# Kernel tuning notes

Measured on AMD Instinct MI355X. Metric: run time of the kernel, lower is better.

## Reference

```python
import jax, jax.numpy as jnp
import numpy as np

B, T, D = 4, 1024, 2048      # batch, tokens, d_model (= Linear out_features)
N, S, H = 8, 8, 8            # n_concepts, gate_rank, degen_rank
ETA = 1.0


def setup_inputs() -> dict:
    key = jax.random.key(0)
    ks = jax.random.split(key, 9)
    return {
        "x": jax.random.normal(ks[0], (B, T, D), jnp.float32),
        # selector params (kaiming-ish then / d_model^2 -> small); use /D for nontrivial values
        "select_weight": jax.random.normal(ks[1], (N, D, S), jnp.float32) / D,
        "select_mean_diff": jax.random.normal(ks[2], (N, D), jnp.float32) / D,
        "imp_center": jax.random.normal(ks[3], (N,), jnp.float32),
        "imp_slope": jax.random.normal(ks[4], (N,), jnp.float32) * 5.0,
        "lora_update": jax.random.normal(ks[5], (N, D, H), jnp.float32) * 0.02,
        "lora_degen": jax.random.normal(ks[6], (N, D, H), jnp.float32) * 0.02,
        "bias_w": jax.random.normal(ks[7], (N, D), jnp.float32) * 0.02,
        "debias_w": jax.random.normal(ks[8], (N, D), jnp.float32) * 0.02,
    }


def reference(x, select_weight, select_mean_diff, imp_center, imp_slope,
              lora_update, lora_degen, bias_w, debias_w):
    # ---- SimpleSelectorOutProp ----
    # x: [B,T,D]; x_diff: [B,N,T,D]  (x.unsqueeze(1) - mean_diff[None,:,None,:])
    x_diff = x[:, None, :, :] - select_mean_diff[None, :, None, :]
    x_diff = x_diff / jnp.linalg.norm(x_diff, axis=3, keepdims=True)
    # cont: [B,N,T,S] = einsum('nds,bntd->bnts')**2
    cont = jnp.einsum('nds,bntd->bnts', select_weight, x_diff) ** 2
    score = cont.sum(axis=-1)                                   # [B,N,T]
    gate = jax.nn.sigmoid(imp_slope[None, :, None] * (score - imp_center[None, :, None]))
    sel_scale = gate.max(axis=1)[..., None]                     # [B,T,1] (max over concepts)
    sel_idx = gate.argmax(axis=1)                               # [B,T] int (top-1 concept)

    # ---- top-1 concept gather + low-rank update ----
    debias = jnp.take(debias_w, sel_idx, axis=0)                # [B,T,D]
    bias = jnp.take(bias_w, sel_idx, axis=0)                    # [B,T,D]
    upd = jnp.take(lora_update, sel_idx, axis=0)                # [B,T,D,H]
    dgn = jnp.take(lora_degen, sel_idx, axis=0)                 # [B,T,D,H]

    x_debias = x - debias
    mod_x = jnp.einsum('btdh,btd->bth', upd, x_debias)          # [B,T,H]
    degen_up = jnp.einsum('btdh,bth->btd', dgn, mod_x)          # [B,T,D]
    mod_x_bias = ETA * (bias + degen_up)

    # gated residual blend: (1 - s) * x + s * mod_x_bias
    return (1.0 - sel_scale) * x + sel_scale * mod_x_bias
```

## Files before the change

### kernel.cpp

```cpp
#include <hip/hip_runtime.h>
#include <math.h>

typedef unsigned short u16;
typedef unsigned int   u32;
typedef unsigned long long u64;
typedef __attribute__((ext_vector_type(4))) unsigned short u16x4;
typedef __attribute__((ext_vector_type(8))) unsigned short bf16x8;
typedef __attribute__((ext_vector_type(8))) short sh8;
typedef __attribute__((ext_vector_type(4))) float f32x4;

#define BT     4096
#define D      2048
#define NC     8
#define NCOL   144
#define KSPLIT 8
#define KR     (D / KSPLIT)

__device__ __forceinline__ float bf2f(u16 v) {
    u32 u = ((u32)v) << 16;
    float f; __builtin_memcpy(&f, &u, 4); return f;
}
__device__ __forceinline__ u16 f2bf(float f) {
    u32 u; __builtin_memcpy(&u, &f, 4);
    u += 0x7fffu + ((u >> 16) & 1);
    return (u16)(u >> 16);
}

__device__ __forceinline__ int detect_fp32(const void* xv) {
    const u16* p = (const u16*)xv;
    int l = threadIdx.x & 63;
    bool bad = false;
#pragma unroll
    for (int i = 0; i < 4; i++) {
        float v = bf2f(p[l * 4 + i]);
        if (!(fabsf(v) < 1e4f)) bad = true;
    }
    return __ballot(bad) != 0ull;
}

template<int DT> struct IO;
template<> struct IO<0> {
    static __device__ __forceinline__ float ld1(const void* p, size_t i) {
        return bf2f(((const u16*)p)[i]);
    }
    static __device__ __forceinline__ void ld4(const void* p, size_t i, float* o) {
        u16x4 v = *(const u16x4*)((const u16*)p + i);
#pragma unroll
        for (int k = 0; k < 4; k++) o[k] = bf2f(v[k]);
    }
    static __device__ __forceinline__ void ld8(const void* p, size_t i, float* o) {
        bf16x8 v = *(const bf16x8*)((const u16*)p + i);
#pragma unroll
        for (int k = 0; k < 8; k++) o[k] = bf2f(v[k]);
    }
    static __device__ __forceinline__ void st4(void* p, size_t i, const float* v) {
        u16x4 o;
#pragma unroll
        for (int k = 0; k < 4; k++) o[k] = f2bf(v[k]);
        *(u16x4*)((u16*)p + i) = o;
    }
    static __device__ __forceinline__ u16 ldbf(const void* p, size_t i) {
        return ((const u16*)p)[i];
    }
    static __device__ __forceinline__ sh8 afrag(const void* p, size_t i) {
        return *(const sh8*)((const u16*)p + i);
    }
};
template<> struct IO<1> {
    static __device__ __forceinline__ float ld1(const void* p, size_t i) {
        return ((const float*)p)[i];
    }
    static __device__ __forceinline__ void ld4(const void* p, size_t i, float* o) {
        f32x4 a = *(const f32x4*)((const float*)p + i);
#pragma unroll
        for (int k = 0; k < 4; k++) o[k] = a[k];
    }
    static __device__ __forceinline__ void ld8(const void* p, size_t i, float* o) {
        f32x4 a = *(const f32x4*)((const float*)p + i);
        f32x4 b = *(const f32x4*)((const float*)p + i + 4);
#pragma unroll
        for (int k = 0; k < 4; k++) { o[k] = a[k]; o[4 + k] = b[k]; }
    }
    static __device__ __forceinline__ void st4(void* p, size_t i, const float* v) {
        f32x4 a;
#pragma unroll
        for (int k = 0; k < 4; k++) a[k] = v[k];
        *(f32x4*)((float*)p + i) = a;
    }
    static __device__ __forceinline__ u16 ldbf(const void* p, size_t i) {
        return f2bf(((const float*)p)[i]);
    }
    static __device__ __forceinline__ sh8 afrag(const void* p, size_t i) {
        f32x4 a = *(const f32x4*)((const float*)p + i);
        f32x4 b = *(const f32x4*)((const float*)p + i + 4);
        sh8 r;
#pragma unroll
        for (int k = 0; k < 4; k++) {
            r[k]     = (short)f2bf(a[k]);
            r[4 + k] = (short)f2bf(b[k]);
        }
        return r;
    }
};

template<int DT>
__device__ __forceinline__ void prep_part(const void* selW, const void* upd,
                                          const void* mu, u16* __restrict__ WtT) {
    int idx = blockIdx.x * 256 + threadIdx.x;
    int j = idx >> 8, d0 = (idx & 255) * 8;
    bf16x8 v;
    if (j < 64) {
        int n = j >> 3, s = j & 7;
#pragma unroll
        for (int i = 0; i < 8; i++) v[i] = IO<DT>::ldbf(selW, ((size_t)n * D + d0 + i) * 8 + s);
    } else if (j < 128) {
        int n = (j - 64) >> 3, h = j & 7;
#pragma unroll
        for (int i = 0; i < 8; i++) v[i] = IO<DT>::ldbf(upd, ((size_t)n * D + d0 + i) * 8 + h);
    } else if (j < 136) {
#pragma unroll
        for (int i = 0; i < 8; i++) v[i] = IO<DT>::ldbf(mu, (size_t)(j - 128) * D + d0 + i);
    } else {
#pragma unroll
        for (int i = 0; i < 8; i++) v[i] = 0;
    }
    *(bf16x8*)(WtT + (size_t)j * D + d0) = v;
}

template<int DT>
__device__ __forceinline__ void consts_part(const void* W, const void* mu,
                                            const void* upd, const void* deb,
                                            float* gOff, float* gMu2, float* gUb) {
    int bid = blockIdx.x - 144;
    int n = bid >> 3, t = threadIdx.x;
    int d = (bid & 7) * 256 + t;

    float mud = IO<DT>::ld1(mu,  (size_t)n * D + d);
    float dbd = IO<DT>::ld1(deb, (size_t)n * D + d);
    float m2 = mud * mud;
    float wv[8], uv[8], o[8], u[8];
    IO<DT>::ld8(W,   ((size_t)n * D + d) * 8, wv);
    IO<DT>::ld8(upd, ((size_t)n * D + d) * 8, uv);
#pragma unroll
    for (int s = 0; s < 8; s++) { o[s] = wv[s] * mud; u[s] = uv[s] * dbd; }

#pragma unroll
    for (int i = 1; i < 64; i <<= 1) {
        m2 += __shfl_xor(m2, i, 64);
#pragma unroll
        for (int s = 0; s < 8; s++) {
            o[s] += __shfl_xor(o[s], i, 64);
            u[s] += __shfl_xor(u[s], i, 64);
        }
    }
    __shared__ float red[4][17];
    int wave = t >> 6, lane = t & 63;
    if (lane == 0) {
        red[wave][0] = m2;
#pragma unroll
        for (int s = 0; s < 8; s++) { red[wave][1 + s] = o[s]; red[wave][9 + s] = u[s]; }
    }
    __syncthreads();
    if (t < 17) {
        float acc = red[0][t] + red[1][t] + red[2][t] + red[3][t];
        if (t == 0)      atomicAdd(&gMu2[n], acc);
        else if (t < 9)  atomicAdd(&gOff[n * 8 + t - 1], acc);
        else             atomicAdd(&gUb[n * 8 + t - 9], acc);
    }
}

template<int DT>
__device__ __forceinline__ void dgnb_part(const void* dgn, u16* __restrict__ dgnb) {
    int idx = (blockIdx.x - 208) * 256 + threadIdx.x;
    float v[8];
    IO<DT>::ld8(dgn, (size_t)idx * 8, v);
    bf16x8 o;
#pragma unroll
    for (int k = 0; k < 8; k++) o[k] = f2bf(v[k]);
    *(bf16x8*)(dgnb + (size_t)idx * 8) = o;
}

__global__ __launch_bounds__(256) void k_prep(
    const void* x, const void* selW, const void* upd, const void* mu,
    const void* deb, const void* dgn, u16* WtT,
    float* gOff, float* gMu2, float* gUb, u16* dgnb) {
    int f = detect_fp32(x);
    if (blockIdx.x < 144) {
        if (f) prep_part<1>(selW, upd, mu, WtT); else prep_part<0>(selW, upd, mu, WtT);
    } else if (blockIdx.x < 208) {
        if (f) consts_part<1>(selW, mu, upd, deb, gOff, gMu2, gUb);
        else   consts_part<0>(selW, mu, upd, deb, gOff, gMu2, gUb);
    } else {
        if (f) dgnb_part<1>(dgn, dgnb); else dgnb_part<0>(dgn, dgnb);
    }
}

template<int DT>
__device__ __forceinline__ void gemm_body(const void* X, const u16* __restrict__ WtT,
                                          float* __restrict__ Pslices,
                                          float* __restrict__ sumx2p) {
    const int t = threadIdx.x;
    const int w = t >> 6, l = t & 63;
    const int m = l & 15, q = l >> 4;
    const int tok0 = blockIdx.x * 64 + w * 16;
    const int p = blockIdx.y;
    const int k0 = p * KR;

    const size_t aoff = (size_t)(tok0 + m) * D + k0 + q * 8;
    const u16* bp = WtT + (size_t)m * D + k0 + q * 8;

    f32x4 acc[9];
#pragma unroll
    for (int ct = 0; ct < 9; ct++) acc[ct] = (f32x4){0.f, 0.f, 0.f, 0.f};
    float s2 = 0.f;

#pragma unroll 2
    for (int ks = 0; ks < KR / 32; ks++) {
        sh8 a = IO<DT>::afrag(X, aoff + ks * 32);
        sh8 b[9];
#pragma unroll
        for (int ct = 0; ct < 9; ct++)
            b[ct] = *(const sh8*)(bp + (size_t)ct * 16 * D + ks * 32);
#pragma unroll
        for (int i = 0; i < 8; i++) {
            float xv = bf2f((u16)a[i]);
            s2 = fmaf(xv, xv, s2);
        }
#pragma unroll
        for (int ct = 0; ct < 9; ct++)
            acc[ct] = __builtin_amdgcn_mfma_f32_16x16x32_bf16(a, b[ct], acc[ct], 0, 0, 0);
    }

    s2 += __shfl_xor(s2, 16, 64);
    s2 += __shfl_xor(s2, 32, 64);
    if (l < 16) sumx2p[(size_t)p * BT + tok0 + l] = s2;

    float* Ps = Pslices + (size_t)p * BT * NCOL;
#pragma unroll
    for (int ct = 0; ct < 9; ct++)
#pragma unroll
        for (int r = 0; r < 4; r++)
            Ps[(size_t)(tok0 + q * 4 + r) * NCOL + ct * 16 + m] = acc[ct][r];
}
__global__ __launch_bounds__(256) void k_gemm(const void* X, const u16* WtT,
                                              float* Pslices, float* sumx2p) {
    if (detect_fp32(X)) gemm_body<1>(X, WtT, Pslices, sumx2p);
    else                gemm_body<0>(X, WtT, Pslices, sumx2p);
}

template<int DT>
__device__ __forceinline__ void gate_body(
    const float* __restrict__ Pslices, const float* __restrict__ sumx2p,
    const void* CENTER, const void* SLOPE,
    const float* __restrict__ OFF, const float* __restrict__ MU2,
    const float* __restrict__ UB,
    float* __restrict__ svals, int* __restrict__ cs, float* __restrict__ mxs) {
    const int g = blockIdx.x * 256 + threadIdx.x;
    const int tok = g >> 3, n = g & 7;

    f32x4 pa = {0.f, 0.f, 0.f, 0.f}, pb = {0.f, 0.f, 0.f, 0.f};
    float mdot = 0.f, s2 = 0.f;
#pragma unroll
    for (int p = 0; p < KSPLIT; p++) {
        const float* pr = Pslices + ((size_t)p * BT + tok) * NCOL;
        f32x4 a = *(const f32x4*)(pr + 8 * n);
        f32x4 b = *(const f32x4*)(pr + 8 * n + 4);
#pragma unroll
        for (int k = 0; k < 4; k++) { pa[k] += a[k]; pb[k] += b[k]; }
        mdot += pr[128 + n];
        s2 += sumx2p[(size_t)p * BT + tok];
    }

    float norm2 = s2 - 2.f * mdot + MU2[n];
    float sc = 0.f;
#pragma unroll
    for (int s = 0; s < 4; s++) {
        float d0 = pa[s] - OFF[8 * n + s];
        float d1 = pb[s] - OFF[8 * n + 4 + s];
        sc += d0 * d0 + d1 * d1;
    }
    sc /= norm2;
    float zv = IO<DT>::ld1(SLOPE, n) * (sc - IO<DT>::ld1(CENTER, n));
    int iv = n;
#pragma unroll
    for (int i = 1; i < 8; i <<= 1) {
        float z2 = __shfl_xor(zv, i, 64);
        int   i2 = __shfl_xor(iv, i, 64);
        if (z2 > zv || (z2 == zv && i2 < iv)) { zv = z2; iv = i2; }
    }
    const int c = iv;
    float mxv = 0.f;
#pragma unroll
    for (int p = 0; p < KSPLIT; p++)
        mxv += Pslices[((size_t)p * BT + tok) * NCOL + 64 + 8 * c + n];
    mxs[(size_t)tok * 8 + n] = mxv - UB[c * 8 + n];
    if (n == 0) { svals[tok] = 1.f / (1.f + expf(-zv)); cs[tok] = c; }
}
__global__ __launch_bounds__(256) void k_gate(
    const float* Pslices, const float* sumx2p, const void* X,
    const void* CENTER, const void* SLOPE,
    const float* OFF, const float* MU2, const float* UB,
    float* svals, int* cs, float* mxs) {
    if (detect_fp32(X)) gate_body<1>(Pslices, sumx2p, CENTER, SLOPE, OFF, MU2, UB, svals, cs, mxs);
    else                gate_body<0>(Pslices, sumx2p, CENTER, SLOPE, OFF, MU2, UB, svals, cs, mxs);
}

template<int DT>
__device__ __forceinline__ void blend_body(
    const void* X, const float* __restrict__ svals, const int* __restrict__ cs,
    const float* __restrict__ mxs, const u16* __restrict__ DGNB,
    const void* BIAS, void* OUT) {
    const int tok = blockIdx.x >> 1;
    const int d0 = (blockIdx.x & 1) * 1024 + threadIdx.x * 4;

    const int c = cs[tok];
    const float sval = svals[tok];
    f32x4 mxa = *(const f32x4*)(mxs + (size_t)tok * 8);
    f32x4 mxb = *(const f32x4*)(mxs + (size_t)tok * 8 + 4);

    float xf[4], bv[4], ov[4];
    IO<DT>::ld4(X,    (size_t)tok * D + d0, xf);
    IO<DT>::ld4(BIAS, (size_t)c * D + d0, bv);
#pragma unroll
    for (int i = 0; i < 4; i++) {
        bf16x8 v = *(const bf16x8*)(DGNB + ((size_t)c * D + d0 + i) * 8);
        float du = bf2f(v[0]) * mxa[0] + bf2f(v[1]) * mxa[1]
                 + bf2f(v[2]) * mxa[2] + bf2f(v[3]) * mxa[3]
                 + bf2f(v[4]) * mxb[0] + bf2f(v[5]) * mxb[1]
                 + bf2f(v[6]) * mxb[2] + bf2f(v[7]) * mxb[3];
        ov[i] = (1.f - sval) * xf[i] + sval * (bv[i] + du);
    }
    IO<DT>::st4(OUT, (size_t)tok * D + d0, ov);
}
__global__ __launch_bounds__(256) void k_blend(
    const void* X, const float* svals, const int* cs, const float* mxs,
    const u16* DGNB, const void* BIAS, void* OUT) {
    if (detect_fp32(X)) blend_body<1>(X, svals, cs, mxs, DGNB, BIAS, OUT);
    else                blend_body<0>(X, svals, cs, mxs, DGNB, BIAS, OUT);
}

extern "C" void kernel_launch(void* const* d_in, const int* in_sizes, int n_in,
                              void* d_out, int out_size, void* d_ws, size_t ws_size,
                              hipStream_t stream) {
    const void* x      = d_in[0];
    const void* selW   = d_in[1];
    const void* mu     = d_in[2];
    const void* center = d_in[3];
    const void* slope  = d_in[4];
    const void* upd    = d_in[5];
    const void* dgn    = d_in[6];
    const void* biasW  = d_in[7];
    const void* debW   = d_in[8];

    float* Pslices = (float*)d_out;
    char* ws = (char*)d_ws;
    float* sumx2p = (float*)ws;
    float* svals  = (float*)(ws + 131072);
    int*   cs     = (int*)  (ws + 147456);
    float* mxs    = (float*)(ws + 163840);
    u16*   WtT    = (u16*)  (ws + 294912);
    u16*   dgnb   = (u16*)  (ws + 884736);
    float* consts = (float*)(ws + 1146880);
    float* off = consts, *mu2 = consts + 64, *ub = consts + 72;

    hipMemsetAsync(consts, 0, 576, stream);
    k_prep <<<272, 256, 0, stream>>>(x, selW, upd, mu, debW, dgn,
                                     WtT, off, mu2, ub, dgnb);
    k_gemm <<<dim3(BT / 64, KSPLIT), 256, 0, stream>>>(x, WtT, Pslices, sumx2p);
    k_gate <<<BT * NC / 256, 256, 0, stream>>>(Pslices, sumx2p, x, center, slope,
                                               off, mu2, ub, svals, cs, mxs);
    k_blend<<<BT * 2, 256, 0, stream>>>(x, svals, cs, mxs, dgnb, biasW, d_out);
}
```

Baseline: 143.4 us.

## Fuse gate into blend, store partial GEMM results as bf16, double K-split

```diff
diff --git a/kernel.cpp b/kernel.cpp
--- a/kernel.cpp
+++ b/kernel.cpp
@@ -13,7 +13,7 @@
 #define D      2048
 #define NC     8
 #define NCOL   144
-#define KSPLIT 8
+#define KSPLIT 16
 #define KR     (D / KSPLIT)
 
 __device__ __forceinline__ float bf2f(u16 v) {
@@ -131,19 +131,22 @@
 __device__ __forceinline__ void consts_part(const void* W, const void* mu,
                                             const void* upd, const void* deb,
                                             float* gOff, float* gMu2, float* gUb) {
-    int bid = blockIdx.x - 144;
-    int n = bid >> 3, t = threadIdx.x;
-    int d = (bid & 7) * 256 + t;
-
-    float mud = IO<DT>::ld1(mu,  (size_t)n * D + d);
-    float dbd = IO<DT>::ld1(deb, (size_t)n * D + d);
-    float m2 = mud * mud;
-    float wv[8], uv[8], o[8], u[8];
-    IO<DT>::ld8(W,   ((size_t)n * D + d) * 8, wv);
-    IO<DT>::ld8(upd, ((size_t)n * D + d) * 8, uv);
-#pragma unroll
-    for (int s = 0; s < 8; s++) { o[s] = wv[s] * mud; u[s] = uv[s] * dbd; }
-
+    int n = blockIdx.x - 144, t = threadIdx.x;
+    float o[8] = {}, u[8] = {};
+    float m2 = 0.f;
+    for (int d = t; d < D; d += 256) {
+        float mud = IO<DT>::ld1(mu,  (size_t)n * D + d);
+        float dbd = IO<DT>::ld1(deb, (size_t)n * D + d);
+        m2 += mud * mud;
+        float wv[8], uv[8];
+        IO<DT>::ld8(W,   ((size_t)n * D + d) * 8, wv);
+        IO<DT>::ld8(upd, ((size_t)n * D + d) * 8, uv);
+#pragma unroll
+        for (int s = 0; s < 8; s++) {
+            o[s] += wv[s] * mud;
+            u[s] += uv[s] * dbd;
+        }
+    }
 #pragma unroll
     for (int i = 1; i < 64; i <<= 1) {
         m2 += __shfl_xor(m2, i, 64);
@@ -161,17 +164,20 @@
         for (int s = 0; s < 8; s++) { red[wave][1 + s] = o[s]; red[wave][9 + s] = u[s]; }
     }
     __syncthreads();
-    if (t < 17) {
-        float acc = red[0][t] + red[1][t] + red[2][t] + red[3][t];
-        if (t == 0)      atomicAdd(&gMu2[n], acc);
-        else if (t < 9)  atomicAdd(&gOff[n * 8 + t - 1], acc);
-        else             atomicAdd(&gUb[n * 8 + t - 9], acc);
+    if (t == 0) {
+        float acc[17];
+#pragma unroll
+        for (int i = 0; i < 17; i++)
+            acc[i] = red[0][i] + red[1][i] + red[2][i] + red[3][i];
+        gMu2[n] = acc[0];
+#pragma unroll
+        for (int s = 0; s < 8; s++) { gOff[n * 8 + s] = acc[1 + s]; gUb[n * 8 + s] = acc[9 + s]; }
     }
 }
 
 template<int DT>
 __device__ __forceinline__ void dgnb_part(const void* dgn, u16* __restrict__ dgnb) {
-    int idx = (blockIdx.x - 208) * 256 + threadIdx.x;
+    int idx = (blockIdx.x - 152) * 256 + threadIdx.x;
     float v[8];
     IO<DT>::ld8(dgn, (size_t)idx * 8, v);
     bf16x8 o;
@@ -187,7 +193,7 @@
     int f = detect_fp32(x);
     if (blockIdx.x < 144) {
         if (f) prep_part<1>(selW, upd, mu, WtT); else prep_part<0>(selW, upd, mu, WtT);
-    } else if (blockIdx.x < 208) {
+    } else if (blockIdx.x < 152) {
         if (f) consts_part<1>(selW, mu, upd, deb, gOff, gMu2, gUb);
         else   consts_part<0>(selW, mu, upd, deb, gOff, gMu2, gUb);
     } else {
@@ -197,7 +203,7 @@
 
 template<int DT>
 __device__ __forceinline__ void gemm_body(const void* X, const u16* __restrict__ WtT,
-                                          float* __restrict__ Pslices,
+                                          u16* __restrict__ Pb,
                                           float* __restrict__ sumx2p) {
     const int t = threadIdx.x;
     const int w = t >> 6, l = t & 63;
@@ -214,7 +220,7 @@
     for (int ct = 0; ct < 9; ct++) acc[ct] = (f32x4){0.f, 0.f, 0.f, 0.f};
     float s2 = 0.f;
 
-#pragma unroll 2
+#pragma unroll
     for (int ks = 0; ks < KR / 32; ks++) {
         sh8 a = IO<DT>::afrag(X, aoff + ks * 32);
         sh8 b[9];
@@ -235,108 +241,169 @@
     s2 += __shfl_xor(s2, 32, 64);
     if (l < 16) sumx2p[(size_t)p * BT + tok0 + l] = s2;
 
-    float* Ps = Pslices + (size_t)p * BT * NCOL;
+    u16* Ps = Pb + (size_t)p * BT * NCOL;
 #pragma unroll
     for (int ct = 0; ct < 9; ct++)
 #pragma unroll
         for (int r = 0; r < 4; r++)
-            Ps[(size_t)(tok0 + q * 4 + r) * NCOL + ct * 16 + m] = acc[ct][r];
+            Ps[(size_t)(tok0 + q * 4 + r) * NCOL + ct * 16 + m] = f2bf(acc[ct][r]);
 }
 __global__ __launch_bounds__(256) void k_gemm(const void* X, const u16* WtT,
-                                              float* Pslices, float* sumx2p) {
-    if (detect_fp32(X)) gemm_body<1>(X, WtT, Pslices, sumx2p);
-    else                gemm_body<0>(X, WtT, Pslices, sumx2p);
-}
-
-template<int DT>
-__device__ __forceinline__ void gate_body(
-    const float* __restrict__ Pslices, const float* __restrict__ sumx2p,
-    const void* CENTER, const void* SLOPE,
+                                              u16* Pb, float* sumx2p) {
+    if (detect_fp32(X)) gemm_body<1>(X, WtT, Pb, sumx2p);
+    else                gemm_body<0>(X, WtT, Pb, sumx2p);
+}
+
+template<int DT>
+__device__ __forceinline__ void gate_wave(
+    const u16* __restrict__ Pb, const float* __restrict__ sumx2p,
+    int tok, int l, const void* CENTER, const void* SLOPE,
     const float* __restrict__ OFF, const float* __restrict__ MU2,
     const float* __restrict__ UB,
-    float* __restrict__ svals, int* __restrict__ cs, float* __restrict__ mxs) {
-    const int g = blockIdx.x * 256 + threadIdx.x;
-    const int tok = g >> 3, n = g & 7;
-
-    f32x4 pa = {0.f, 0.f, 0.f, 0.f}, pb = {0.f, 0.f, 0.f, 0.f};
-    float mdot = 0.f, s2 = 0.f;
-#pragma unroll
-    for (int p = 0; p < KSPLIT; p++) {
-        const float* pr = Pslices + ((size_t)p * BT + tok) * NCOL;
-        f32x4 a = *(const f32x4*)(pr + 8 * n);
-        f32x4 b = *(const f32x4*)(pr + 8 * n + 4);
-#pragma unroll
-        for (int k = 0; k < 4; k++) { pa[k] += a[k]; pb[k] += b[k]; }
-        mdot += pr[128 + n];
-        s2 += sumx2p[(size_t)p * BT + tok];
-    }
-
-    float norm2 = s2 - 2.f * mdot + MU2[n];
-    float sc = 0.f;
-#pragma unroll
-    for (int s = 0; s < 4; s++) {
-        float d0 = pa[s] - OFF[8 * n + s];
-        float d1 = pb[s] - OFF[8 * n + 4 + s];
-        sc += d0 * d0 + d1 * d1;
-    }
-    sc /= norm2;
-    float zv = IO<DT>::ld1(SLOPE, n) * (sc - IO<DT>::ld1(CENTER, n));
-    int iv = n;
+    float* sval_out, int* c_out, float* mx_out) {
+    const int n = l & 7, p2 = l >> 3;
+    float pa[8] = {};
+    float mdot = 0.f;
+#pragma unroll
+    for (int pp = 0; pp < 2; pp++) {
+        const u16* pr = Pb + ((size_t)(2 * p2 + pp) * BT + tok) * NCOL;
+        bf16x8 v = *(const bf16x8*)(pr + 8 * n);
+#pragma unroll
+        for (int k = 0; k < 8; k++) pa[k] += bf2f(v[k]);
+        mdot += bf2f(pr[128 + n]);
+    }
+#pragma unroll
+    for (int i = 8; i < 64; i <<= 1) {
+#pragma unroll
+        for (int k = 0; k < 8; k++) pa[k] += __shfl_xor(pa[k], i, 64);
+        mdot += __shfl_xor(mdot, i, 64);
+    }
+    float s2 = sumx2p[(size_t)(l & 15) * BT + tok];
+#pragma unroll
+    for (int i = 1; i < 16; i <<= 1) s2 += __shfl_xor(s2, i, 64);
+
+    float zv = -1e30f; int iv = n;
+    if (l < 8) {
+        float norm2 = s2 - 2.f * mdot + MU2[n];
+        float sc = 0.f;
+#pragma unroll
+        for (int s = 0; s < 8; s++) {
+            float dg = pa[s] - OFF[8 * n + s];
+            sc += dg * dg;
+        }
+        sc /= norm2;
+        zv = IO<DT>::ld1(SLOPE, n) * (sc - IO<DT>::ld1(CENTER, n));
+    }
 #pragma unroll
     for (int i = 1; i < 8; i <<= 1) {
         float z2 = __shfl_xor(zv, i, 64);
         int   i2 = __shfl_xor(iv, i, 64);
         if (z2 > zv || (z2 == zv && i2 < iv)) { zv = z2; iv = i2; }
     }
-    const int c = iv;
+    const int c = __shfl(iv, 0, 64);
+    const float zbest = __shfl(zv, 0, 64);
+
     float mxv = 0.f;
 #pragma unroll
-    for (int p = 0; p < KSPLIT; p++)
-        mxv += Pslices[((size_t)p * BT + tok) * NCOL + 64 + 8 * c + n];
-    mxs[(size_t)tok * 8 + n] = mxv - UB[c * 8 + n];
-    if (n == 0) { svals[tok] = 1.f / (1.f + expf(-zv)); cs[tok] = c; }
+    for (int pp = 0; pp < 2; pp++)
+        mxv += bf2f(Pb[((size_t)(2 * p2 + pp) * BT + tok) * NCOL + 64 + 8 * c + n]);
+#pragma unroll
+    for (int i = 8; i < 64; i <<= 1) mxv += __shfl_xor(mxv, i, 64);
+
+    *sval_out = 1.f / (1.f + expf(-zbest));
+    *c_out = c;
+    *mx_out = mxv - UB[c * 8 + n];
+}
+
+template<int DT>
+__device__ __forceinline__ void kgate_body(
+    const u16* Pb, const float* sumx2p, const void* CENTER, const void* SLOPE,
+    const float* OFF, const float* MU2, const float* UB,
+    float* svals, int* cs, float* mxs) {
+    const int w = threadIdx.x >> 6, l = threadIdx.x & 63;
+    const int tok = blockIdx.x * 4 + w;
+    float sval, mxv; int c;
+    gate_wave<DT>(Pb, sumx2p, tok, l, CENTER, SLOPE, OFF, MU2, UB, &sval, &c, &mxv);
+    if (l < 8) mxs[(size_t)tok * 8 + l] = mxv;
+    if (l == 0) { svals[tok] = sval; cs[tok] = c; }
 }
 __global__ __launch_bounds__(256) void k_gate(
-    const float* Pslices, const float* sumx2p, const void* X,
+    const void* X, const u16* Pb, const float* sumx2p,
     const void* CENTER, const void* SLOPE,
     const float* OFF, const float* MU2, const float* UB,
     float* svals, int* cs, float* mxs) {
-    if (detect_fp32(X)) gate_body<1>(Pslices, sumx2p, CENTER, SLOPE, OFF, MU2, UB, svals, cs, mxs);
-    else                gate_body<0>(Pslices, sumx2p, CENTER, SLOPE, OFF, MU2, UB, svals, cs, mxs);
+    if (detect_fp32(X)) kgate_body<1>(Pb, sumx2p, CENTER, SLOPE, OFF, MU2, UB, svals, cs, mxs);
+    else                kgate_body<0>(Pb, sumx2p, CENTER, SLOPE, OFF, MU2, UB, svals, cs, mxs);
 }
 
 template<int DT>
 __device__ __forceinline__ void blend_body(
-    const void* X, const float* __restrict__ svals, const int* __restrict__ cs,
-    const float* __restrict__ mxs, const u16* __restrict__ DGNB,
-    const void* BIAS, void* OUT) {
-    const int tok = blockIdx.x >> 1;
-    const int d0 = (blockIdx.x & 1) * 1024 + threadIdx.x * 4;
-
-    const int c = cs[tok];
-    const float sval = svals[tok];
-    f32x4 mxa = *(const f32x4*)(mxs + (size_t)tok * 8);
-    f32x4 mxb = *(const f32x4*)(mxs + (size_t)tok * 8 + 4);
-
-    float xf[4], bv[4], ov[4];
-    IO<DT>::ld4(X,    (size_t)tok * D + d0, xf);
-    IO<DT>::ld4(BIAS, (size_t)c * D + d0, bv);
-#pragma unroll
-    for (int i = 0; i < 4; i++) {
-        bf16x8 v = *(const bf16x8*)(DGNB + ((size_t)c * D + d0 + i) * 8);
-        float du = bf2f(v[0]) * mxa[0] + bf2f(v[1]) * mxa[1]
-                 + bf2f(v[2]) * mxa[2] + bf2f(v[3]) * mxa[3]
-                 + bf2f(v[4]) * mxb[0] + bf2f(v[5]) * mxb[1]
-                 + bf2f(v[6]) * mxb[2] + bf2f(v[7]) * mxb[3];
-        ov[i] = (1.f - sval) * xf[i] + sval * (bv[i] + du);
-    }
-    IO<DT>::st4(OUT, (size_t)tok * D + d0, ov);
+    const void* X, const u16* __restrict__ Pb, const float* __restrict__ sumx2p,
+    const void* CENTER, const void* SLOPE,
+    const float* __restrict__ OFF, const float* __restrict__ MU2,
+    const float* __restrict__ UB,
+    const float* __restrict__ svals, const int* __restrict__ cs,
+    const float* __restrict__ mxs,
+    const u16* __restrict__ DGNB, const void* BIAS, void* OUT, int fused) {
+    const int tok = blockIdx.x;
+    const int t = threadIdx.x, w = t >> 6, l = t & 63;
+    __shared__ float sm[10];
+    __shared__ int smc;
+
+    float xf0[4], xf1[4];
+    IO<DT>::ld4(X, (size_t)tok * D + t * 4, xf0);
+    IO<DT>::ld4(X, (size_t)tok * D + 1024 + t * 4, xf1);
+
+    if (w == 0) {
+        float sval, mxv; int c;
+        if (fused) {
+            gate_wave<DT>(Pb, sumx2p, tok, l, CENTER, SLOPE, OFF, MU2, UB,
+                          &sval, &c, &mxv);
+        } else {
+            sval = svals[tok]; c = cs[tok];
+            mxv = (l < 8) ? mxs[(size_t)tok * 8 + l] : 0.f;
+        }
+        if (l < 8) sm[2 + l] = mxv;
+        if (l == 0) { sm[0] = sval; smc = c; }
+    }
+    __syncthreads();
+
+    const float sval = sm[0];
+    const int c = smc;
+    float mx[8];
+#pragma unroll
+    for (int h = 0; h < 8; h++) mx[h] = sm[2 + h];
+
+#pragma unroll
+    for (int half = 0; half < 2; half++) {
+        const int d0 = half * 1024 + t * 4;
+        const float* xf = half ? xf1 : xf0;
+        float bv[4], ov[4];
+        IO<DT>::ld4(BIAS, (size_t)c * D + d0, bv);
+#pragma unroll
+        for (int i = 0; i < 4; i++) {
+            bf16x8 v = *(const bf16x8*)(DGNB + ((size_t)c * D + d0 + i) * 8);
+            float du = bf2f(v[0]) * mx[0] + bf2f(v[1]) * mx[1]
+                     + bf2f(v[2]) * mx[2] + bf2f(v[3]) * mx[3]
+                     + bf2f(v[4]) * mx[4] + bf2f(v[5]) * mx[5]
+                     + bf2f(v[6]) * mx[6] + bf2f(v[7]) * mx[7];
+            ov[i] = (1.f - sval) * xf[i] + sval * (bv[i] + du);
+        }
+        IO<DT>::st4(OUT, (size_t)tok * D + d0, ov);
+    }
 }
 __global__ __launch_bounds__(256) void k_blend(
-    const void* X, const float* svals, const int* cs, const float* mxs,
-    const u16* DGNB, const void* BIAS, void* OUT) {
-    if (detect_fp32(X)) blend_body<1>(X, svals, cs, mxs, DGNB, BIAS, OUT);
-    else                blend_body<0>(X, svals, cs, mxs, DGNB, BIAS, OUT);
+    const void* X, const u16* Pb, const float* sumx2p,
+    const void* CENTER, const void* SLOPE,
+    const float* OFF, const float* MU2, const float* UB,
+    const float* svals, const int* cs, const float* mxs,
+    const u16* DGNB, const void* BIAS, void* OUT, int fused) {
+    if (detect_fp32(X))
+        blend_body<1>(X, Pb, sumx2p, CENTER, SLOPE, OFF, MU2, UB,
+                      svals, cs, mxs, DGNB, BIAS, OUT, fused);
+    else
+        blend_body<0>(X, Pb, sumx2p, CENTER, SLOPE, OFF, MU2, UB,
+                      svals, cs, mxs, DGNB, BIAS, OUT, fused);
 }
 
 extern "C" void kernel_launch(void* const* d_in, const int* in_sizes, int n_in,
@@ -352,22 +419,38 @@
     const void* biasW  = d_in[7];
     const void* debW   = d_in[8];
 
-    float* Pslices = (float*)d_out;
+    const size_t o_sumx2 = 0;
+    const size_t o_wtt   = 262144;
+    const size_t o_dgnb  = o_wtt + 589824;
+    const size_t o_const = o_dgnb + 262144;
+    const size_t o_sv    = o_const + 1024;
+    const size_t o_cs    = o_sv + 16384;
+    const size_t o_mxs   = o_cs + 16384;
+    const size_t o_pb    = o_mxs + 131072;
+    const size_t need    = o_pb + (size_t)KSPLIT * BT * NCOL * 2;
+
     char* ws = (char*)d_ws;
-    float* sumx2p = (float*)ws;
-    float* svals  = (float*)(ws + 131072);
-    int*   cs     = (int*)  (ws + 147456);
-    float* mxs    = (float*)(ws + 163840);
-    u16*   WtT    = (u16*)  (ws + 294912);
-    u16*   dgnb   = (u16*)  (ws + 884736);
-    float* consts = (float*)(ws + 1146880);
-    float* off = consts, *mu2 = consts + 64, *ub = consts + 72;
-
-    hipMemsetAsync(consts, 0, 576, stream);
-    k_prep <<<272, 256, 0, stream>>>(x, selW, upd, mu, debW, dgn,
-                                     WtT, off, mu2, ub, dgnb);
-    k_gemm <<<dim3(BT / 64, KSPLIT), 256, 0, stream>>>(x, WtT, Pslices, sumx2p);
-    k_gate <<<BT * NC / 256, 256, 0, stream>>>(Pslices, sumx2p, x, center, slope,
-                                               off, mu2, ub, svals, cs, mxs);
-    k_blend<<<BT * 2, 256, 0, stream>>>(x, svals, cs, mxs, dgnb, biasW, d_out);
-}
+    float* sumx2p = (float*)(ws + o_sumx2);
+    u16*   WtT    = (u16*)(ws + o_wtt);
+    u16*   dgnb   = (u16*)(ws + o_dgnb);
+    float* consts = (float*)(ws + o_const);
+    float* svals  = (float*)(ws + o_sv);
+    int*   cs     = (int*)(ws + o_cs);
+    float* mxs    = (float*)(ws + o_mxs);
+    float* off = consts;
+    float* mu2 = consts + 64;
+    float* ub  = consts + 72;
+
+    const int fused = (ws_size >= need) ? 1 : 0;
+    u16* Pb = fused ? (u16*)(ws + o_pb) : (u16*)d_out;
+
+    k_prep<<<216, 256, 0, stream>>>(x, selW, upd, mu, debW, dgn,
+                                    WtT, off, mu2, ub, dgnb);
+    k_gemm<<<dim3(BT / 64, KSPLIT), 256, 0, stream>>>(x, WtT, Pb, sumx2p);
+    if (!fused)
+        k_gate<<<BT / 4, 256, 0, stream>>>(x, Pb, sumx2p, center, slope,
+                                           off, mu2, ub, svals, cs, mxs);
+    k_blend<<<BT, 256, 0, stream>>>(x, Pb, sumx2p, center, slope,
+                                    off, mu2, ub, svals, cs, mxs,
+                                    dgnb, biasW, d_out, fused);
+}
```

Measured after the change: 151.1 us. 1.05x slower.
